# Optimization experiments

Hardware: AMD Instinct MI355X
Metric: run time of the kernel (lower is better)

Reference implementation:

```python
import jax, jax.numpy as jnp
import numpy as np

N_E = 8192
E_DIM = 64
BETA = 0.25
N_TOKENS = 32768


def setup_inputs() -> dict:
    key = jax.random.key(0)
    k1, k2 = jax.random.split(key)
    x = jax.random.normal(k1, (N_TOKENS, E_DIM), dtype=jnp.float32)
    # nn.Embedding weight initialized uniform(-1/n_e, 1/n_e)
    codebook = jax.random.uniform(k2, (N_E, E_DIM), dtype=jnp.float32,
                                  minval=-1.0 / N_E, maxval=1.0 / N_E)
    return {"x": x, "codebook": codebook, "start": 0, "end": N_E, "use_sk": 0}


def reference(x, codebook, start, end, use_sk):
    # use_sk=0 -> argmin branch (sinkhorn branch calls external helper, not exercised)
    latent = x.reshape(-1, E_DIM)                       # [N, D]
    cb = codebook[start:end]                            # [K, D]
    # squared euclidean distances: ||z||^2 + ||e||^2 - 2 z.e
    d = (jnp.sum(latent * latent, axis=1, keepdims=True)
         + jnp.sum(cb * cb, axis=1)[None, :]
         - 2.0 * jnp.einsum('nd,kd->nk', latent, cb))   # [N, K]
    indices = jnp.argmin(d, axis=-1) + start            # [N]
    x_q = codebook[indices].reshape(x.shape)            # gather
    sg = jax.lax.stop_gradient
    commitment_loss = jnp.mean((sg(x_q) - x) ** 2)
    codebook_loss = jnp.mean((x_q - sg(x)) ** 2)
    loss = codebook_loss + BETA * commitment_loss
    x_q_st = x + sg(x_q - x)                            # straight-through estimator
    indices = indices.reshape(x.shape[:-1])
    return x_q_st, loss, indices
```

## Files before the change

kernel.cpp:

```cpp
#include <hip/hip_runtime.h>
#include <math.h>


#define N_E    8192
#define EDIM   64
#define NTOK   32768
#define NELEM  (NTOK * EDIM)
#define CSZ    32
#define NCHUNK (N_E / CSZ)
#define WINDOW 3e-4f
#define KEXT   80
#define TTOK   256
#define TCODE  2048
#define SROW   88

typedef __attribute__((ext_vector_type(8)))  short          short8;
typedef __attribute__((ext_vector_type(8)))  unsigned short ushort8v;
typedef __attribute__((ext_vector_type(4)))  unsigned short ushort4v;
typedef __attribute__((ext_vector_type(16))) float          f32x16;

__device__ __forceinline__ unsigned short f2bf(float f) {
  unsigned int u = __float_as_uint(f);
  return (unsigned short)((u + 0x7FFFu + ((u >> 16) & 1u)) >> 16);
}
__device__ __forceinline__ unsigned short f2h(float f) {
  union { _Float16 h; unsigned short u; } cv; cv.h = (_Float16)f; return cv.u;
}
__device__ __forceinline__ float h2f(unsigned short b) {
  union { _Float16 h; unsigned short u; } cv; cv.u = b; return (float)cv.h;
}

__device__ __forceinline__ unsigned long long vq_eval_pack(
    const float* __restrict__ cb, int k, const float4* __restrict__ xl4,
    float sx, const float* __restrict__ sc) {
#pragma clang fp contract(off)
  const float4* c4 = (const float4*)(cb + (size_t)k * EDIM);
  float t[8];
#pragma unroll
  for (int j = 0; j < 8; ++j) t[j] = 0.0f;
#pragma unroll
  for (int i = 0; i < 8; ++i) {
    float4 cA4 = c4[2*i], cB4 = c4[2*i+1];
    float4 pA = xl4[2*i], pB = xl4[2*i+1];
    t[0] += cA4.x * pA.x; t[1] += cA4.y * pA.y;
    t[2] += cA4.z * pA.z; t[3] += cA4.w * pA.w;
    t[4] += cB4.x * pB.x; t[5] += cB4.y * pB.y;
    t[6] += cB4.z * pB.z; t[7] += cB4.w * pB.w;
  }
  float tt = ((t[0]+t[1]) + (t[2]+t[3])) + ((t[4]+t[5]) + (t[6]+t[7]));
  float d = (sx + sc[k]) - 2.0f * tt;
  unsigned int db = __float_as_uint(d);
  unsigned int en = db ^ ((unsigned int)((int)db >> 31) | 0x80000000u);
  return ((unsigned long long)en << 32) | (unsigned int)k;
}

__global__ __launch_bounds__(256) void vq_sc(const float* __restrict__ cb,
                                             float* __restrict__ sc,
                                             unsigned short* __restrict__ cbf) {
#pragma clang fp contract(off)
  int r = blockIdx.x * 256 + threadIdx.x;
  const float4* c4 = (const float4*)(cb + (size_t)r * EDIM);
  float a[8];
#pragma unroll
  for (int j = 0; j < 8; ++j) a[j] = 0.0f;
#pragma unroll
  for (int i = 0; i < 8; ++i) {
    float4 pA = c4[2*i], pB = c4[2*i+1];
    a[0] += pA.x * pA.x; a[1] += pA.y * pA.y; a[2] += pA.z * pA.z; a[3] += pA.w * pA.w;
    a[4] += pB.x * pB.x; a[5] += pB.y * pB.y; a[6] += pB.z * pB.z; a[7] += pB.w * pB.w;
  }
  float sval = ((a[0]+a[1]) + (a[2]+a[3])) + ((a[4]+a[5]) + (a[6]+a[7]));
  sc[r] = sval;
  unsigned short* dst = cbf + (size_t)r * KEXT;
#pragma unroll
  for (int h = 0; h < 8; ++h) {
    float4 fA = c4[2*h], fB = c4[2*h+1];
    ushort8v o = {f2bf(fA.x), f2bf(fA.y), f2bf(fA.z), f2bf(fA.w),
                  f2bf(fB.x), f2bf(fB.y), f2bf(fB.z), f2bf(fB.w)};
    *(ushort8v*)&dst[h * 8] = o;
  }
  ushort8v t0 = {0,0,0,0,0,0,0,0};
  t0[0] = f2bf(sval);
  *(ushort8v*)&dst[64] = t0;
  ushort8v z = {0,0,0,0,0,0,0,0};
  *(ushort8v*)&dst[72] = z;
}

__global__ __launch_bounds__(256, 2) void vq_pass1(
    const float* __restrict__ x, const unsigned short* __restrict__ cbf,
    unsigned short* __restrict__ minima,
    const int* __restrict__ p_start, const int* __restrict__ p_end) {
  __shared__ unsigned short Xs[TTOK * SROW];
  __shared__ unsigned short Cs[128 * SROW];
  int tid = threadIdx.x;
  int tb = blockIdx.x;
  int cbk = blockIdx.y;
  int s = *p_start, e = *p_end;

  const float4* xg = (const float4*)(x + (size_t)tb * TTOK * EDIM);
#pragma unroll
  for (int p = 0; p < 16; ++p) {
    int idx = tid + p * 256;
    int row = idx >> 4, c4i = idx & 15;
    float4 f = xg[idx];
    ushort4v o = {f2bf(f.x), f2bf(f.y), f2bf(f.z), f2bf(f.w)};
    *(ushort4v*)&Xs[row * SROW + c4i * 4] = o;
  }
  {
    ushort8v t0 = {0,0,0,0,0,0,0,0};
    t0[0] = f2bf(-0.5f);
    ushort8v z = {0,0,0,0,0,0,0,0};
    *(ushort8v*)&Xs[tid * SROW + 64] = t0;
    *(ushort8v*)&Xs[tid * SROW + 72] = z;
  }
  const ushort8v* cg0 = (const ushort8v*)(cbf + (size_t)cbk * TCODE * KEXT);
#pragma unroll
  for (int p = 0; p < 5; ++p) {
    int idx = tid + p * 256;
    int row = idx / 10, h = idx % 10;
    *(ushort8v*)&Cs[row * SROW + h * 8] = cg0[idx];
  }
  __syncthreads();

  int lane = tid & 63, wv = tid >> 6;
  int half = lane >> 5, ln = lane & 31;
  int tokbase = wv * 64;
  short8 bfr[2][5];
#pragma unroll
  for (int tg = 0; tg < 2; ++tg)
#pragma unroll
    for (int ks = 0; ks < 5; ++ks)
      bfr[tg][ks] = *(const short8*)&Xs[(tokbase + tg*32 + ln) * SROW + ks*16 + half*8];

  int token = tb * TTOK + tokbase + lane;
  unsigned short* rowp = minima + (size_t)token * NCHUNK + cbk * 64;

  for (int nbg = 0; nbg < 4; ++nbg) {
    unsigned pk8[8];
#pragma unroll
    for (int ni = 0; ni < 4; ++ni) {
      int nb = nbg * 4 + ni;
      ushort8v creg[5];
      if (nb < 15) {
        const ushort8v* cg =
            (const ushort8v*)(cbf + ((size_t)cbk * TCODE + (nb + 1) * 128) * KEXT);
#pragma unroll
        for (int p = 0; p < 5; ++p) creg[p] = cg[tid + p * 256];
      }
      f32x16 acc[2][4];
#pragma unroll
      for (int tg = 0; tg < 2; ++tg)
#pragma unroll
        for (int ct = 0; ct < 4; ++ct) acc[tg][ct] = (f32x16)0.0f;
#pragma unroll
      for (int ks = 0; ks < 5; ++ks)
#pragma unroll
        for (int ct = 0; ct < 4; ++ct) {
          short8 a = *(const short8*)&Cs[(ct*32 + ln) * SROW + ks*16 + half*8];
          acc[0][ct] = __builtin_amdgcn_mfma_f32_32x32x16_bf16(a, bfr[0][ks],
                                                               acc[0][ct], 0, 0, 0);
          acc[1][ct] = __builtin_amdgcn_mfma_f32_32x32x16_bf16(a, bfr[1][ks],
                                                               acc[1][ct], 0, 0, 0);
        }
      __syncthreads();
      if (nb < 15) {
#pragma unroll
        for (int p = 0; p < 5; ++p) {
          int idx = tid + p * 256;
          int row = idx / 10, h = idx % 10;
          *(ushort8v*)&Cs[row * SROW + h * 8] = creg[p];
        }
      }
      int cbase0 = cbk * TCODE + nb * 128;
      bool full = (cbase0 >= s) && (cbase0 + 128 <= e);
      float cm[4];
#pragma unroll
      for (int ct = 0; ct < 4; ++ct) {
        float v0 = -INFINITY, v1 = -INFINITY;
        if (full) {
#pragma unroll
          for (int r = 0; r < 16; ++r) {
            v0 = fmaxf(v0, acc[0][ct][r]);
            v1 = fmaxf(v1, acc[1][ct][r]);
          }
        } else {
          int c0 = cbase0 + ct * 32;
#pragma unroll
          for (int r = 0; r < 16; ++r) {
            int code = c0 + (r & 3) + 8 * (r >> 2) + 4 * half;
            if (code >= s && code < e) {
              v0 = fmaxf(v0, acc[0][ct][r]);
              v1 = fmaxf(v1, acc[1][ct][r]);
            }
          }
        }
        v0 = fmaxf(v0, __shfl_xor(v0, 32, 64));
        v1 = fmaxf(v1, __shfl_xor(v1, 32, 64));
        cm[ct] = half ? v1 : v0;
      }
      pk8[ni*2]     = (unsigned)f2h(-2.0f * cm[0])
                    | ((unsigned)f2h(-2.0f * cm[1]) << 16);
      pk8[ni*2 + 1] = (unsigned)f2h(-2.0f * cm[2])
                    | ((unsigned)f2h(-2.0f * cm[3]) << 16);
      __syncthreads();
    }
    uint4 w0, w1;
    w0.x = pk8[0]; w0.y = pk8[1]; w0.z = pk8[2]; w0.w = pk8[3];
    w1.x = pk8[4]; w1.y = pk8[5]; w1.z = pk8[6]; w1.w = pk8[7];
    *(uint4*)(rowp + nbg * 16)     = w0;
    *(uint4*)(rowp + nbg * 16 + 8) = w1;
  }
}

__global__ __launch_bounds__(256) void vq_rescue(
    const float* __restrict__ x, const float* __restrict__ cb,
    const float* __restrict__ sc, const unsigned short* __restrict__ minima,
    float* __restrict__ out_xq, float* __restrict__ out_idx,
    float* __restrict__ partial,
    const int* __restrict__ p_start, const int* __restrict__ p_end) {
#pragma clang fp contract(off)
  __shared__ float xs[4][64];
  __shared__ float sdata[4];
  int tid  = threadIdx.x;
  int wv   = tid >> 6;
  int lane = tid & 63;
  int token = blockIdx.x * 4 + wv;

  float xx = x[(size_t)token * EDIM + lane];
  xs[wv][lane] = xx;
  __syncthreads();
  const float4* xl4 = (const float4*)xs[wv];

  float a[8];
#pragma unroll
  for (int j = 0; j < 8; ++j) a[j] = 0.0f;
#pragma unroll
  for (int i = 0; i < 8; ++i) {
    float4 pA = xl4[2*i], pB = xl4[2*i+1];
    a[0] += pA.x * pA.x; a[1] += pA.y * pA.y; a[2] += pA.z * pA.z; a[3] += pA.w * pA.w;
    a[4] += pB.x * pB.x; a[5] += pB.y * pB.y; a[6] += pB.z * pB.z; a[7] += pB.w * pB.w;
  }
  float sx = ((a[0]+a[1]) + (a[2]+a[3])) + ((a[4]+a[5]) + (a[6]+a[7]));

  uint2 u2 = *(const uint2*)(minima + (size_t)token * NCHUNK + lane * 4);
  float mv[4] = {h2f((unsigned short)(u2.x & 0xFFFFu)),
                 h2f((unsigned short)(u2.x >> 16)),
                 h2f((unsigned short)(u2.y & 0xFFFFu)),
                 h2f((unsigned short)(u2.y >> 16))};
  float m = fminf(fminf(mv[0], mv[1]), fminf(mv[2], mv[3]));
#pragma unroll
  for (int off = 32; off >= 1; off >>= 1) m = fminf(m, __shfl_xor(m, off, 64));
  float thr = m + WINDOW;
  unsigned long long fmask[4];
#pragma unroll
  for (int cc = 0; cc < 4; ++cc) fmask[cc] = __ballot(mv[cc] <= thr);

  int s = *p_start, e = *p_end;
  unsigned long long bestpack = ~0ull;
  int half = lane >> 5;
  int pend = -1;

#pragma unroll 1
  for (int cc = 0; cc < 5; ++cc) {
    unsigned long long fm = (cc < 4) ? fmask[cc] : 0ull;
    while (fm || (cc == 4 && pend >= 0)) {
      int cA, cB;
      if (cc == 4) { cA = pend; cB = -1; pend = -2; }
      else {
        int b = __ffsll((long long)fm) - 1; fm &= fm - 1;
        int c = b * 4 + cc;
        if (pend < 0) { pend = c; continue; }
        cA = pend; cB = c; pend = -1;
      }
      int ch = half ? cB : cA;
      if (ch >= 0) {
        int k = ch * CSZ + (lane & 31);
        if (k >= s && k < e) {
          unsigned long long pk = vq_eval_pack(cb, k, xl4, sx, sc);
          if (pk < bestpack) bestpack = pk;
        }
      }
      if (pend == -2) { pend = -1; break; }
    }
  }
#pragma unroll
  for (int off = 32; off >= 1; off >>= 1) {
    unsigned long long o = __shfl_xor(bestpack, off, 64);
    if (o < bestpack) bestpack = o;
  }
  int bidx = (int)(unsigned int)(bestpack & 0xFFFFFFFFull);

  float qv = cb[(size_t)bidx * EDIM + lane];
  float diff = qv - xx;
  out_xq[(size_t)token * EDIM + lane] = xx + diff;
  if (lane == 0) out_idx[token] = (float)bidx;

  float l = diff * diff;
#pragma unroll
  for (int off = 32; off >= 1; off >>= 1) l += __shfl_down(l, off, 64);
  if (lane == 0) sdata[wv] = l;
  __syncthreads();
  if (tid == 0)
    partial[blockIdx.x] = (sdata[0] + sdata[1]) + (sdata[2] + sdata[3]);
}

__global__ __launch_bounds__(256) void vq_loss(const float* __restrict__ partial,
                                               float* __restrict__ out_loss) {
  int tid = threadIdx.x;
  float s = 0.0f;
  for (int i = tid; i < NTOK / 4; i += 256) s += partial[i];
#pragma unroll
  for (int off = 32; off >= 1; off >>= 1) s += __shfl_down(s, off, 64);
  __shared__ float sdata[4];
  if ((tid & 63) == 0) sdata[tid >> 6] = s;
  __syncthreads();
  if (tid == 0) {
    float total = (sdata[0] + sdata[1]) + (sdata[2] + sdata[3]);
    float m = total * (1.0f / (float)NELEM);
    out_loss[0] = m + 0.25f * m;
  }
}

extern "C" void kernel_launch(void* const* d_in, const int* in_sizes, int n_in,
                              void* d_out, int out_size, void* d_ws, size_t ws_size,
                              hipStream_t stream) {
  const float* x  = (const float*)d_in[0];
  const float* cb = (const float*)d_in[1];
  const int* p_start = (const int*)d_in[2];
  const int* p_end   = (const int*)d_in[3];

  float* ws = (float*)d_ws;
  float* sc      = ws;
  float* partial = ws + N_E;
  unsigned short* cbf = (unsigned short*)(ws + 2 * N_E);
  unsigned short* minima = cbf + (size_t)N_E * KEXT;

  float* out      = (float*)d_out;
  float* out_xq   = out;
  float* out_loss = out + NELEM;
  float* out_idx  = out + NELEM + 1;

  vq_sc<<<N_E / 256, 256, 0, stream>>>(cb, sc, cbf);
  dim3 g1(NTOK / TTOK, N_E / TCODE);
  vq_pass1<<<g1, 256, 0, stream>>>(x, cbf, minima, p_start, p_end);
  vq_rescue<<<NTOK / 4, 256, 0, stream>>>(x, cb, sc, minima, out_xq, out_idx,
                                          partial, p_start, p_end);
  vq_loss<<<1, 256, 0, stream>>>(partial, out_loss);
}
```

Baseline: 219.0 us.

## Emit per-chunk candidate bitmasks in pass1 to prune fp32 rescue evaluations

Pass1 now computes, for each 32-code chunk, a bitmask of the codes whose bf16 score falls within a small window (AWIN) of the chunk maximum and writes it to a new workspace buffer. The rescue kernel reads these masks and re-evaluates in fp32 only the flagged codes of the qualifying chunks, instead of all 32 codes of every chunk within WINDOW. This cuts rescue arithmetic and codebook reads at the cost of extra comparison work and a 32 MB mask write in pass1. It also risks missing the true argmin if the bf16 ranking error exceeds AWIN.

Result: slower. 242.5 us (+10.8%).

```diff
diff --git a/kernel.cpp b/kernel.cpp
--- a/kernel.cpp
+++ b/kernel.cpp
@@ -9,6 +9,7 @@
 #define CSZ    32
 #define NCHUNK (N_E / CSZ)
 #define WINDOW 3e-4f
+#define AWIN   1.5e-4f
 #define KEXT   80
 #define TTOK   256
 #define TCODE  2048
@@ -88,7 +89,7 @@
 
 __global__ __launch_bounds__(256, 2) void vq_pass1(
     const float* __restrict__ x, const unsigned short* __restrict__ cbf,
-    unsigned short* __restrict__ minima,
+    unsigned short* __restrict__ minima, unsigned int* __restrict__ maskb,
     const int* __restrict__ p_start, const int* __restrict__ p_end) {
   __shared__ unsigned short Xs[TTOK * SROW];
   __shared__ unsigned short Cs[128 * SROW];
@@ -134,9 +135,11 @@
 
   int token = tb * TTOK + tokbase + lane;
   unsigned short* rowp = minima + (size_t)token * NCHUNK + cbk * 64;
+  unsigned int*   mrow = maskb  + (size_t)token * NCHUNK + cbk * 64;
 
   for (int nbg = 0; nbg < 4; ++nbg) {
     unsigned pk8[8];
+    unsigned mk[16];
 #pragma unroll
     for (int ni = 0; ni < 4; ++ni) {
       int nb = nbg * 4 + ni;
@@ -176,6 +179,7 @@
       float cm[4];
 #pragma unroll
       for (int ct = 0; ct < 4; ++ct) {
+        int c0 = cbase0 + ct * 32;
         float v0 = -INFINITY, v1 = -INFINITY;
         if (full) {
 #pragma unroll
@@ -184,7 +188,6 @@
             v1 = fmaxf(v1, acc[1][ct][r]);
           }
         } else {
-          int c0 = cbase0 + ct * 32;
 #pragma unroll
           for (int r = 0; r < 16; ++r) {
             int code = c0 + (r & 3) + 8 * (r >> 2) + 4 * half;
@@ -197,6 +200,27 @@
         v0 = fmaxf(v0, __shfl_xor(v0, 32, 64));
         v1 = fmaxf(v1, __shfl_xor(v1, 32, 64));
         cm[ct] = half ? v1 : v0;
+        float t0 = v0 - AWIN, t1 = v1 - AWIN;
+        unsigned b0 = 0, b1 = 0;
+        if (full) {
+#pragma unroll
+          for (int r = 0; r < 16; ++r) {
+            int pos = (r & 3) + 8 * (r >> 2) + 4 * half;
+            if (acc[0][ct][r] >= t0) b0 |= (1u << pos);
+            if (acc[1][ct][r] >= t1) b1 |= (1u << pos);
+          }
+        } else {
+#pragma unroll
+          for (int r = 0; r < 16; ++r) {
+            int pos = (r & 3) + 8 * (r >> 2) + 4 * half;
+            bool ok = (c0 + pos >= s) && (c0 + pos < e);
+            if (ok && acc[0][ct][r] >= t0) b0 |= (1u << pos);
+            if (ok && acc[1][ct][r] >= t1) b1 |= (1u << pos);
+          }
+        }
+        b0 |= __shfl_xor(b0, 32, 64);
+        b1 |= __shfl_xor(b1, 32, 64);
+        mk[ni * 4 + ct] = half ? b1 : b0;
       }
       pk8[ni*2]     = (unsigned)f2h(-2.0f * cm[0])
                     | ((unsigned)f2h(-2.0f * cm[1]) << 16);
@@ -209,12 +233,22 @@
     w1.x = pk8[4]; w1.y = pk8[5]; w1.z = pk8[6]; w1.w = pk8[7];
     *(uint4*)(rowp + nbg * 16)     = w0;
     *(uint4*)(rowp + nbg * 16 + 8) = w1;
+    uint4 m0, m1, m2, m3;
+    m0.x = mk[0];  m0.y = mk[1];  m0.z = mk[2];  m0.w = mk[3];
+    m1.x = mk[4];  m1.y = mk[5];  m1.z = mk[6];  m1.w = mk[7];
+    m2.x = mk[8];  m2.y = mk[9];  m2.z = mk[10]; m2.w = mk[11];
+    m3.x = mk[12]; m3.y = mk[13]; m3.z = mk[14]; m3.w = mk[15];
+    *(uint4*)(mrow + nbg * 16)      = m0;
+    *(uint4*)(mrow + nbg * 16 + 4)  = m1;
+    *(uint4*)(mrow + nbg * 16 + 8)  = m2;
+    *(uint4*)(mrow + nbg * 16 + 12) = m3;
   }
 }
 
 __global__ __launch_bounds__(256) void vq_rescue(
     const float* __restrict__ x, const float* __restrict__ cb,
     const float* __restrict__ sc, const unsigned short* __restrict__ minima,
+    const unsigned int* __restrict__ maskb,
     float* __restrict__ out_xq, float* __restrict__ out_idx,
     float* __restrict__ partial,
     const int* __restrict__ p_start, const int* __restrict__ p_end) {
@@ -251,36 +285,27 @@
 #pragma unroll
   for (int off = 32; off >= 1; off >>= 1) m = fminf(m, __shfl_xor(m, off, 64));
   float thr = m + WINDOW;
-  unsigned long long fmask[4];
-#pragma unroll
-  for (int cc = 0; cc < 4; ++cc) fmask[cc] = __ballot(mv[cc] <= thr);
 
   int s = *p_start, e = *p_end;
   unsigned long long bestpack = ~0ull;
-  int half = lane >> 5;
-  int pend = -1;
-
+
+  bool anyf = (mv[0] <= thr) | (mv[1] <= thr) | (mv[2] <= thr) | (mv[3] <= thr);
+  if (anyf) {
+    uint4 mq = *(const uint4*)(maskb + (size_t)token * NCHUNK + lane * 4);
+    unsigned mks[4] = {mq.x, mq.y, mq.z, mq.w};
 #pragma unroll 1
-  for (int cc = 0; cc < 5; ++cc) {
-    unsigned long long fm = (cc < 4) ? fmask[cc] : 0ull;
-    while (fm || (cc == 4 && pend >= 0)) {
-      int cA, cB;
-      if (cc == 4) { cA = pend; cB = -1; pend = -2; }
-      else {
-        int b = __ffsll((long long)fm) - 1; fm &= fm - 1;
-        int c = b * 4 + cc;
-        if (pend < 0) { pend = c; continue; }
-        cA = pend; cB = c; pend = -1;
-      }
-      int ch = half ? cB : cA;
-      if (ch >= 0) {
-        int k = ch * CSZ + (lane & 31);
+    for (int cc = 0; cc < 4; ++cc) {
+      if (!(mv[cc] <= thr)) continue;
+      unsigned msk = mks[cc];
+      while (msk) {
+        int j = __ffs(msk) - 1;
+        msk &= msk - 1;
+        int k = (lane * 4 + cc) * CSZ + j;
         if (k >= s && k < e) {
           unsigned long long pk = vq_eval_pack(cb, k, xl4, sx, sc);
           if (pk < bestpack) bestpack = pk;
         }
       }
-      if (pend == -2) { pend = -1; break; }
     }
   }
 #pragma unroll
@@ -334,6 +359,7 @@
   float* partial = ws + N_E;
   unsigned short* cbf = (unsigned short*)(ws + 2 * N_E);
   unsigned short* minima = cbf + (size_t)N_E * KEXT;
+  unsigned int*   maskb  = (unsigned int*)(minima + (size_t)NTOK * NCHUNK);
 
   float* out      = (float*)d_out;
   float* out_xq   = out;
@@ -342,8 +368,8 @@
 
   vq_sc<<<N_E / 256, 256, 0, stream>>>(cb, sc, cbf);
   dim3 g1(NTOK / TTOK, N_E / TCODE);
-  vq_pass1<<<g1, 256, 0, stream>>>(x, cbf, minima, p_start, p_end);
-  vq_rescue<<<NTOK / 4, 256, 0, stream>>>(x, cb, sc, minima, out_xq, out_idx,
+  vq_pass1<<<g1, 256, 0, stream>>>(x, cbf, minima, maskb, p_start, p_end);
+  vq_rescue<<<NTOK / 4, 256, 0, stream>>>(x, cb, sc, minima, maskb, out_xq, out_idx,
                                           partial, p_start, p_end);
   vq_loss<<<1, 256, 0, stream>>>(partial, out_loss);
 }
```
